# Performance work log

Hardware: AMD Instinct MI355X
Metric: run time of the kernel (lower is better)

The kernel has to match this reference:

```python
import jax, jax.numpy as jnp
import numpy as np

N, NU, R, NX, NY = 16384, 2, 256, 8, 2


def setup_inputs() -> dict:
    key = jax.random.key(0)
    ks = jax.random.split(key, 10)
    A = jax.random.normal(ks[0], (NX, NX), dtype=jnp.float32)
    # scale A to be stable (spectral radius < 1) so the 16k-step recurrence is well-behaved
    rho = jnp.max(jnp.abs(jnp.linalg.eigvals(A.astype(jnp.float32)))).real
    A = (A * (0.95 / rho)).astype(jnp.float32)
    return {
        "u": jax.random.normal(ks[1], (N, NU, R), dtype=jnp.float32),
        "x0": jax.random.normal(ks[2], (NX, R), dtype=jnp.float32),
        "A": A,
        "B_u": jax.random.normal(ks[3], (NX, NU), dtype=jnp.float32),
        "C_y": jax.random.normal(ks[4], (NY, NX), dtype=jnp.float32),
        "D_yu": jax.random.normal(ks[5], (NY, NU), dtype=jnp.float32),
        "u_mean": jax.random.normal(ks[6], (NU,), dtype=jnp.float32),
        "u_std": jax.random.uniform(ks[7], (NU,), dtype=jnp.float32, minval=0.5, maxval=1.5),
        "y_mean": jax.random.normal(ks[8], (NY,), dtype=jnp.float32),
        "y_std": jax.random.uniform(ks[9], (NY,), dtype=jnp.float32, minval=0.5, maxval=1.5),
    }


def reference(u, x0, A, B_u, C_y, D_yu, u_mean, u_std, y_mean, y_std):
    # normalize input as in _simulate_core
    un = (u - u_mean.reshape(1, -1, 1)) / u_std.reshape(1, -1, 1)  # (N, nu, R)

    def step(x, uk):
        # x: (nx, R), uk: (nu, R)
        y = C_y @ x + D_yu @ uk      # (ny, R)
        x_next = A @ x + B_u @ uk    # (nx, R)
        return x_next, (y, x)

    _, (Y, X) = jax.lax.scan(step, x0, un)  # Y: (N, ny, R), X: (N, nx, R)

    # denormalize output
    y = Y * y_std.reshape(1, -1, 1) + y_mean.reshape(1, -1, 1)
    return y, X
```

## Files before the change

kernel.cpp:

```cpp
#include <hip/hip_runtime.h>


#define NSTEPS 16384
#define NUI 2
#define RB 256
#define NXS 8
#define NYO 2
#define L1 64
#define NC1 (NSTEPS / L1)
#define NC2 (NC1 / 2)

__global__ void pow_k(const float* __restrict__ A,
                      float* __restrict__ A64, float* __restrict__ A128) {
    __shared__ float M[64];
    const int t = threadIdx.x;
    const int i = t >> 3, j = t & 7;
    M[t] = A[t];
    __syncthreads();
    for (int it = 0; it < 6; ++it) {
        float acc = 0.f;
        #pragma unroll
        for (int k = 0; k < 8; ++k) acc += M[i * 8 + k] * M[k * 8 + j];
        __syncthreads();
        M[t] = acc;
        __syncthreads();
    }
    A64[t] = M[t];
    float acc = 0.f;
    #pragma unroll
    for (int k = 0; k < 8; ++k) acc += M[i * 8 + k] * M[k * 8 + j];
    A128[t] = acc;
}

__global__ __launch_bounds__(RB) void phase1_k(
    const float* __restrict__ u, const float* __restrict__ A,
    const float* __restrict__ Bu, const float* __restrict__ um,
    const float* __restrict__ us, float* __restrict__ d64) {
    const int c = blockIdx.x;
    const int r = threadIdx.x;
    float a[NXS][NXS];
    #pragma unroll
    for (int i = 0; i < NXS; ++i)
        #pragma unroll
        for (int j = 0; j < NXS; ++j) a[i][j] = A[i * NXS + j];
    float b0[NXS], b1[NXS];
    #pragma unroll
    for (int i = 0; i < NXS; ++i) { b0[i] = Bu[i * NUI]; b1[i] = Bu[i * NUI + 1]; }
    const float um0 = um[0], um1 = um[1];
    const float is0 = 1.0f / us[0], is1 = 1.0f / us[1];
    float t[NXS];
    #pragma unroll
    for (int i = 0; i < NXS; ++i) t[i] = 0.f;
    const float* up = u + (size_t)c * L1 * NUI * RB + r;
    #pragma unroll 4
    for (int j = 0; j < L1; ++j) {
        const float u0 = (up[0]  - um0) * is0;
        const float u1 = (up[RB] - um1) * is1;
        up += NUI * RB;
        float nt[NXS];
        #pragma unroll
        for (int i = 0; i < NXS; ++i) {
            float acc = fmaf(b0[i], u0, b1[i] * u1);
            #pragma unroll
            for (int k = 0; k < NXS; ++k) acc = fmaf(a[i][k], t[k], acc);
            nt[i] = acc;
        }
        #pragma unroll
        for (int i = 0; i < NXS; ++i) t[i] = nt[i];
    }
    float* dp = d64 + (size_t)c * NXS * RB + r;
    #pragma unroll
    for (int i = 0; i < NXS; ++i) dp[i * RB] = t[i];
}

__global__ __launch_bounds__(RB) void combine_k(
    const float* __restrict__ d64, const float* __restrict__ A64,
    float* __restrict__ d128) {
    const int m = blockIdx.x;
    const int r = threadIdx.x;
    float m64[NXS][NXS];
    #pragma unroll
    for (int i = 0; i < NXS; ++i)
        #pragma unroll
        for (int j = 0; j < NXS; ++j) m64[i][j] = A64[i * NXS + j];
    const float* p0 = d64 + (size_t)(2 * m) * NXS * RB + r;
    const float* p1 = p0 + (size_t)NXS * RB;
    float x[NXS], y[NXS];
    #pragma unroll
    for (int i = 0; i < NXS; ++i) { x[i] = p0[i * RB]; y[i] = p1[i * RB]; }
    float* o = d128 + (size_t)m * NXS * RB + r;
    #pragma unroll
    for (int i = 0; i < NXS; ++i) {
        float acc = y[i];
        #pragma unroll
        for (int k = 0; k < NXS; ++k) acc = fmaf(m64[i][k], x[k], acc);
        o[i * RB] = acc;
    }
}

__global__ __launch_bounds__(RB) void phase2_k(
    const float* __restrict__ x0, const float* __restrict__ A128,
    const float* __restrict__ d128, float* __restrict__ s128) {
    const int r = threadIdx.x;
    float m[NXS][NXS];
    #pragma unroll
    for (int i = 0; i < NXS; ++i)
        #pragma unroll
        for (int j = 0; j < NXS; ++j) m[i][j] = A128[i * NXS + j];
    float s[NXS];
    #pragma unroll
    for (int i = 0; i < NXS; ++i) s[i] = x0[i * RB + r];
    float dA[NXS], dB[NXS];
    #pragma unroll
    for (int i = 0; i < NXS; ++i) dA[i] = d128[i * RB + r];
    #pragma unroll
    for (int i = 0; i < NXS; ++i) dB[i] = d128[(size_t)NXS * RB + i * RB + r];
    for (int c = 0; c < NC2; ++c) {
        float* sp = s128 + (size_t)c * NXS * RB + r;
        #pragma unroll
        for (int i = 0; i < NXS; ++i) sp[i * RB] = s[i];
        float dc[NXS];
        #pragma unroll
        for (int i = 0; i < NXS; ++i) dc[i] = dA[i];
        #pragma unroll
        for (int i = 0; i < NXS; ++i) dA[i] = dB[i];
        if (c + 2 < NC2) {
            const float* dp = d128 + (size_t)(c + 2) * NXS * RB + r;
            #pragma unroll
            for (int i = 0; i < NXS; ++i) dB[i] = dp[i * RB];
        }
        float ns[NXS];
        #pragma unroll
        for (int i = 0; i < NXS; ++i) {
            float acc = dc[i];
            #pragma unroll
            for (int k = 0; k < NXS; ++k) acc = fmaf(m[i][k], s[k], acc);
            ns[i] = acc;
        }
        #pragma unroll
        for (int i = 0; i < NXS; ++i) s[i] = ns[i];
    }
}

__global__ __launch_bounds__(RB) void phase3_k(
    const float* __restrict__ u, const float* __restrict__ s128,
    const float* __restrict__ d64, const float* __restrict__ A64,
    const float* __restrict__ A, const float* __restrict__ Bu,
    const float* __restrict__ Cy, const float* __restrict__ Dyu,
    const float* __restrict__ um, const float* __restrict__ us,
    const float* __restrict__ ym, const float* __restrict__ ys,
    float* __restrict__ Y, float* __restrict__ X) {
    const int c = blockIdx.x;
    const int r = threadIdx.x;
    const int m = c >> 1;
    float a[NXS][NXS];
    #pragma unroll
    for (int i = 0; i < NXS; ++i)
        #pragma unroll
        for (int j = 0; j < NXS; ++j) a[i][j] = A[i * NXS + j];
    float b0[NXS], b1[NXS], c0[NXS], c1[NXS];
    #pragma unroll
    for (int i = 0; i < NXS; ++i) { b0[i] = Bu[i * NUI]; b1[i] = Bu[i * NUI + 1]; }
    #pragma unroll
    for (int k = 0; k < NXS; ++k) { c0[k] = Cy[k]; c1[k] = Cy[NXS + k]; }
    const float d00 = Dyu[0], d01 = Dyu[1], d10 = Dyu[2], d11 = Dyu[3];
    const float um0 = um[0], um1 = um[1];
    const float is0 = 1.0f / us[0], is1 = 1.0f / us[1];
    const float ym0 = ym[0], ym1 = ym[1], ys0 = ys[0], ys1 = ys[1];

    const float* sp = s128 + (size_t)m * NXS * RB + r;
    float sv[NXS];
    #pragma unroll
    for (int i = 0; i < NXS; ++i) sv[i] = sp[i * RB];
    float t[NXS];
    if (c & 1) {
        float m64[NXS][NXS];
        #pragma unroll
        for (int i = 0; i < NXS; ++i)
            #pragma unroll
            for (int j = 0; j < NXS; ++j) m64[i][j] = A64[i * NXS + j];
        const float* dp = d64 + (size_t)(c - 1) * NXS * RB + r;
        #pragma unroll
        for (int i = 0; i < NXS; ++i) {
            float acc = dp[i * RB];
            #pragma unroll
            for (int k = 0; k < NXS; ++k) acc = fmaf(m64[i][k], sv[k], acc);
            t[i] = acc;
        }
    } else {
        #pragma unroll
        for (int i = 0; i < NXS; ++i) t[i] = sv[i];
    }

    const float* up = u + (size_t)c * L1 * NUI * RB + r;
    float* Xp = X + (size_t)c * L1 * NXS * RB + r;
    float* Yp = Y + (size_t)c * L1 * NYO * RB + r;
    #pragma unroll 4
    for (int j = 0; j < L1; ++j) {
        const float u0 = (up[0]  - um0) * is0;
        const float u1 = (up[RB] - um1) * is1;
        up += NUI * RB;
        #pragma unroll
        for (int i = 0; i < NXS; ++i) Xp[i * RB] = t[i];
        Xp += NXS * RB;
        float y0 = fmaf(d00, u0, d01 * u1);
        float y1 = fmaf(d10, u0, d11 * u1);
        #pragma unroll
        for (int k = 0; k < NXS; ++k) {
            y0 = fmaf(c0[k], t[k], y0);
            y1 = fmaf(c1[k], t[k], y1);
        }
        Yp[0]  = fmaf(y0, ys0, ym0);
        Yp[RB] = fmaf(y1, ys1, ym1);
        Yp += NYO * RB;
        float nt[NXS];
        #pragma unroll
        for (int i = 0; i < NXS; ++i) {
            float acc = fmaf(b0[i], u0, b1[i] * u1);
            #pragma unroll
            for (int k = 0; k < NXS; ++k) acc = fmaf(a[i][k], t[k], acc);
            nt[i] = acc;
        }
        #pragma unroll
        for (int i = 0; i < NXS; ++i) t[i] = nt[i];
    }
}

extern "C" void kernel_launch(void* const* d_in, const int* in_sizes, int n_in,
                              void* d_out, int out_size, void* d_ws, size_t ws_size,
                              hipStream_t stream) {
    const float* u   = (const float*)d_in[0];
    const float* x0  = (const float*)d_in[1];
    const float* A   = (const float*)d_in[2];
    const float* Bu  = (const float*)d_in[3];
    const float* Cy  = (const float*)d_in[4];
    const float* Dyu = (const float*)d_in[5];
    const float* um  = (const float*)d_in[6];
    const float* us  = (const float*)d_in[7];
    const float* ym  = (const float*)d_in[8];
    const float* ys  = (const float*)d_in[9];

    float* Y = (float*)d_out;
    float* X = Y + (size_t)NSTEPS * NYO * RB;

    float* ws   = (float*)d_ws;
    float* A64  = ws;
    float* A128 = ws + 64;
    float* d64  = ws + 128;
    float* d128 = d64 + (size_t)NC1 * NXS * RB;
    float* s128 = d128 + (size_t)NC2 * NXS * RB;

    pow_k<<<1, 64, 0, stream>>>(A, A64, A128);
    phase1_k<<<NC1, RB, 0, stream>>>(u, A, Bu, um, us, d64);
    combine_k<<<NC2, RB, 0, stream>>>(d64, A64, d128);
    phase2_k<<<1, RB, 0, stream>>>(x0, A128, d128, s128);
    phase3_k<<<NC1, RB, 0, stream>>>(u, s128, d64, A64, A, Bu, Cy, Dyu,
                                     um, us, ym, ys, Y, X);
}
```

Measured before the change: 269.9 us.

## Shorten scan chunks to 32 steps with 4-way combine and wider serial phase

```diff
diff --git a/kernel.cpp b/kernel.cpp
--- a/kernel.cpp
+++ b/kernel.cpp
@@ -6,18 +6,19 @@
 #define RB 256
 #define NXS 8
 #define NYO 2
-#define L1 64
-#define NC1 (NSTEPS / L1)
-#define NC2 (NC1 / 2)
-
-__global__ void pow_k(const float* __restrict__ A,
-                      float* __restrict__ A64, float* __restrict__ A128) {
-    __shared__ float M[64];
+#define LF 32
+#define NC1 (NSTEPS / LF)
+#define NC2 (NC1 / 4)
+
+__global__ void pow_k(const float* __restrict__ A, float* __restrict__ A32,
+                      float* __restrict__ A64, float* __restrict__ A96,
+                      float* __restrict__ A128) {
+    __shared__ float M[64], T32[64];
     const int t = threadIdx.x;
     const int i = t >> 3, j = t & 7;
     M[t] = A[t];
     __syncthreads();
-    for (int it = 0; it < 6; ++it) {
+    for (int it = 0; it < 5; ++it) {
         float acc = 0.f;
         #pragma unroll
         for (int k = 0; k < 8; ++k) acc += M[i * 8 + k] * M[k * 8 + j];
@@ -25,17 +26,31 @@
         M[t] = acc;
         __syncthreads();
     }
+    T32[t] = M[t];
+    A32[t] = M[t];
+    {
+        float acc = 0.f;
+        #pragma unroll
+        for (int k = 0; k < 8; ++k) acc += M[i * 8 + k] * M[k * 8 + j];
+        __syncthreads();
+        M[t] = acc;
+        __syncthreads();
+    }
     A64[t] = M[t];
-    float acc = 0.f;
-    #pragma unroll
-    for (int k = 0; k < 8; ++k) acc += M[i * 8 + k] * M[k * 8 + j];
-    A128[t] = acc;
+    float a96 = 0.f, a128 = 0.f;
+    #pragma unroll
+    for (int k = 0; k < 8; ++k) {
+        a96  += M[i * 8 + k] * T32[k * 8 + j];
+        a128 += M[i * 8 + k] * M[k * 8 + j];
+    }
+    A96[t] = a96;
+    A128[t] = a128;
 }
 
 __global__ __launch_bounds__(RB) void phase1_k(
     const float* __restrict__ u, const float* __restrict__ A,
     const float* __restrict__ Bu, const float* __restrict__ um,
-    const float* __restrict__ us, float* __restrict__ d64) {
+    const float* __restrict__ us, float* __restrict__ d32) {
     const int c = blockIdx.x;
     const int r = threadIdx.x;
     float a[NXS][NXS];
@@ -51,9 +66,9 @@
     float t[NXS];
     #pragma unroll
     for (int i = 0; i < NXS; ++i) t[i] = 0.f;
-    const float* up = u + (size_t)c * L1 * NUI * RB + r;
+    const float* up = u + (size_t)c * LF * NUI * RB + r;
     #pragma unroll 4
-    for (int j = 0; j < L1; ++j) {
+    for (int j = 0; j < LF; ++j) {
         const float u0 = (up[0]  - um0) * is0;
         const float u1 = (up[RB] - um1) * is1;
         up += NUI * RB;
@@ -68,40 +83,53 @@
         #pragma unroll
         for (int i = 0; i < NXS; ++i) t[i] = nt[i];
     }
-    float* dp = d64 + (size_t)c * NXS * RB + r;
+    float* dp = d32 + (size_t)c * NXS * RB + r;
     #pragma unroll
     for (int i = 0; i < NXS; ++i) dp[i * RB] = t[i];
 }
 
-__global__ __launch_bounds__(RB) void combine_k(
-    const float* __restrict__ d64, const float* __restrict__ A64,
+__global__ __launch_bounds__(RB) void combine4_k(
+    const float* __restrict__ d32, const float* __restrict__ A32,
+    const float* __restrict__ A64, const float* __restrict__ A96,
     float* __restrict__ d128) {
     const int m = blockIdx.x;
     const int r = threadIdx.x;
-    float m64[NXS][NXS];
-    #pragma unroll
-    for (int i = 0; i < NXS; ++i)
-        #pragma unroll
-        for (int j = 0; j < NXS; ++j) m64[i][j] = A64[i * NXS + j];
-    const float* p0 = d64 + (size_t)(2 * m) * NXS * RB + r;
-    const float* p1 = p0 + (size_t)NXS * RB;
-    float x[NXS], y[NXS];
-    #pragma unroll
-    for (int i = 0; i < NXS; ++i) { x[i] = p0[i * RB]; y[i] = p1[i * RB]; }
+    float m32[NXS][NXS], m64[NXS][NXS], m96[NXS][NXS];
+    #pragma unroll
+    for (int i = 0; i < NXS; ++i)
+        #pragma unroll
+        for (int j = 0; j < NXS; ++j) {
+            m32[i][j] = A32[i * NXS + j];
+            m64[i][j] = A64[i * NXS + j];
+            m96[i][j] = A96[i * NXS + j];
+        }
+    const float* p = d32 + (size_t)(4 * m) * NXS * RB + r;
+    float x0[NXS], x1[NXS], x2[NXS], x3[NXS];
+    #pragma unroll
+    for (int i = 0; i < NXS; ++i) {
+        x0[i] = p[i * RB];
+        x1[i] = p[(size_t)NXS * RB + i * RB];
+        x2[i] = p[(size_t)2 * NXS * RB + i * RB];
+        x3[i] = p[(size_t)3 * NXS * RB + i * RB];
+    }
     float* o = d128 + (size_t)m * NXS * RB + r;
     #pragma unroll
     for (int i = 0; i < NXS; ++i) {
-        float acc = y[i];
-        #pragma unroll
-        for (int k = 0; k < NXS; ++k) acc = fmaf(m64[i][k], x[k], acc);
+        float acc = x3[i];
+        #pragma unroll
+        for (int k = 0; k < NXS; ++k) {
+            acc = fmaf(m96[i][k], x0[k], acc);
+            acc = fmaf(m64[i][k], x1[k], acc);
+            acc = fmaf(m32[i][k], x2[k], acc);
+        }
         o[i * RB] = acc;
     }
 }
 
-__global__ __launch_bounds__(RB) void phase2_k(
+__global__ __launch_bounds__(64) void phase2_k(
     const float* __restrict__ x0, const float* __restrict__ A128,
     const float* __restrict__ d128, float* __restrict__ s128) {
-    const int r = threadIdx.x;
+    const int r = blockIdx.x * 64 + threadIdx.x;
     float m[NXS][NXS];
     #pragma unroll
     for (int i = 0; i < NXS; ++i)
@@ -110,41 +138,42 @@
     float s[NXS];
     #pragma unroll
     for (int i = 0; i < NXS; ++i) s[i] = x0[i * RB + r];
-    float dA[NXS], dB[NXS];
-    #pragma unroll
-    for (int i = 0; i < NXS; ++i) dA[i] = d128[i * RB + r];
-    #pragma unroll
-    for (int i = 0; i < NXS; ++i) dB[i] = d128[(size_t)NXS * RB + i * RB + r];
-    for (int c = 0; c < NC2; ++c) {
-        float* sp = s128 + (size_t)c * NXS * RB + r;
-        #pragma unroll
-        for (int i = 0; i < NXS; ++i) sp[i * RB] = s[i];
-        float dc[NXS];
-        #pragma unroll
-        for (int i = 0; i < NXS; ++i) dc[i] = dA[i];
-        #pragma unroll
-        for (int i = 0; i < NXS; ++i) dA[i] = dB[i];
-        if (c + 2 < NC2) {
-            const float* dp = d128 + (size_t)(c + 2) * NXS * RB + r;
-            #pragma unroll
-            for (int i = 0; i < NXS; ++i) dB[i] = dp[i * RB];
-        }
-        float ns[NXS];
-        #pragma unroll
-        for (int i = 0; i < NXS; ++i) {
-            float acc = dc[i];
-            #pragma unroll
-            for (int k = 0; k < NXS; ++k) acc = fmaf(m[i][k], s[k], acc);
-            ns[i] = acc;
-        }
-        #pragma unroll
-        for (int i = 0; i < NXS; ++i) s[i] = ns[i];
+    float P[8][NXS];
+    #pragma unroll
+    for (int sl = 0; sl < 8; ++sl) {
+        const float* dp = d128 + (size_t)sl * NXS * RB + r;
+        #pragma unroll
+        for (int i = 0; i < NXS; ++i) P[sl][i] = dp[i * RB];
+    }
+    for (int c = 0; c < NC2; c += 8) {
+        #pragma unroll
+        for (int sl = 0; sl < 8; ++sl) {
+            const int cc = c + sl;
+            float* sp = s128 + (size_t)cc * NXS * RB + r;
+            #pragma unroll
+            for (int i = 0; i < NXS; ++i) sp[i * RB] = s[i];
+            float ns[NXS];
+            #pragma unroll
+            for (int i = 0; i < NXS; ++i) {
+                float acc = P[sl][i];
+                #pragma unroll
+                for (int k = 0; k < NXS; ++k) acc = fmaf(m[i][k], s[k], acc);
+                ns[i] = acc;
+            }
+            if (cc + 8 < NC2) {
+                const float* dp = d128 + (size_t)(cc + 8) * NXS * RB + r;
+                #pragma unroll
+                for (int i = 0; i < NXS; ++i) P[sl][i] = dp[i * RB];
+            }
+            #pragma unroll
+            for (int i = 0; i < NXS; ++i) s[i] = ns[i];
+        }
     }
 }
 
 __global__ __launch_bounds__(RB) void phase3_k(
     const float* __restrict__ u, const float* __restrict__ s128,
-    const float* __restrict__ d64, const float* __restrict__ A64,
+    const float* __restrict__ d32, const float* __restrict__ A32,
     const float* __restrict__ A, const float* __restrict__ Bu,
     const float* __restrict__ Cy, const float* __restrict__ Dyu,
     const float* __restrict__ um, const float* __restrict__ us,
@@ -152,7 +181,8 @@
     float* __restrict__ Y, float* __restrict__ X) {
     const int c = blockIdx.x;
     const int r = threadIdx.x;
-    const int m = c >> 1;
+    const int m = c >> 2;
+    const int p = c & 3;
     float a[NXS][NXS];
     #pragma unroll
     for (int i = 0; i < NXS; ++i)
@@ -168,40 +198,44 @@
     const float is0 = 1.0f / us[0], is1 = 1.0f / us[1];
     const float ym0 = ym[0], ym1 = ym[1], ys0 = ys[0], ys1 = ys[1];
 
-    const float* sp = s128 + (size_t)m * NXS * RB + r;
-    float sv[NXS];
-    #pragma unroll
-    for (int i = 0; i < NXS; ++i) sv[i] = sp[i * RB];
     float t[NXS];
-    if (c & 1) {
-        float m64[NXS][NXS];
+    {
+        const float* sp = s128 + (size_t)m * NXS * RB + r;
+        #pragma unroll
+        for (int i = 0; i < NXS; ++i) t[i] = sp[i * RB];
+    }
+    if (p) {
+        float a32[NXS][NXS];
         #pragma unroll
         for (int i = 0; i < NXS; ++i)
             #pragma unroll
-            for (int j = 0; j < NXS; ++j) m64[i][j] = A64[i * NXS + j];
-        const float* dp = d64 + (size_t)(c - 1) * NXS * RB + r;
-        #pragma unroll
-        for (int i = 0; i < NXS; ++i) {
-            float acc = dp[i * RB];
-            #pragma unroll
-            for (int k = 0; k < NXS; ++k) acc = fmaf(m64[i][k], sv[k], acc);
-            t[i] = acc;
-        }
-    } else {
-        #pragma unroll
-        for (int i = 0; i < NXS; ++i) t[i] = sv[i];
-    }
-
-    const float* up = u + (size_t)c * L1 * NUI * RB + r;
-    float* Xp = X + (size_t)c * L1 * NXS * RB + r;
-    float* Yp = Y + (size_t)c * L1 * NYO * RB + r;
+            for (int j = 0; j < NXS; ++j) a32[i][j] = A32[i * NXS + j];
+        for (int q = 0; q < p; ++q) {
+            const float* dp = d32 + (size_t)(4 * m + q) * NXS * RB + r;
+            float nt[NXS];
+            #pragma unroll
+            for (int i = 0; i < NXS; ++i) {
+                float acc = dp[i * RB];
+                #pragma unroll
+                for (int k = 0; k < NXS; ++k) acc = fmaf(a32[i][k], t[k], acc);
+                nt[i] = acc;
+            }
+            #pragma unroll
+            for (int i = 0; i < NXS; ++i) t[i] = nt[i];
+        }
+    }
+
+    const float* up = u + (size_t)c * LF * NUI * RB + r;
+    float* Xp = X + (size_t)c * LF * NXS * RB + r;
+    float* Yp = Y + (size_t)c * LF * NYO * RB + r;
     #pragma unroll 4
-    for (int j = 0; j < L1; ++j) {
+    for (int j = 0; j < LF; ++j) {
         const float u0 = (up[0]  - um0) * is0;
         const float u1 = (up[RB] - um1) * is1;
         up += NUI * RB;
         #pragma unroll
-        for (int i = 0; i < NXS; ++i) Xp[i * RB] = t[i];
+        for (int i = 0; i < NXS; ++i)
+            __builtin_nontemporal_store(t[i], Xp + i * RB);
         Xp += NXS * RB;
         float y0 = fmaf(d00, u0, d01 * u1);
         float y1 = fmaf(d10, u0, d11 * u1);
@@ -210,8 +244,8 @@
             y0 = fmaf(c0[k], t[k], y0);
             y1 = fmaf(c1[k], t[k], y1);
         }
-        Yp[0]  = fmaf(y0, ys0, ym0);
-        Yp[RB] = fmaf(y1, ys1, ym1);
+        __builtin_nontemporal_store(fmaf(y0, ys0, ym0), Yp);
+        __builtin_nontemporal_store(fmaf(y1, ys1, ym1), Yp + RB);
         Yp += NYO * RB;
         float nt[NXS];
         #pragma unroll
@@ -244,16 +278,18 @@
     float* X = Y + (size_t)NSTEPS * NYO * RB;
 
     float* ws   = (float*)d_ws;
-    float* A64  = ws;
-    float* A128 = ws + 64;
-    float* d64  = ws + 128;
-    float* d128 = d64 + (size_t)NC1 * NXS * RB;
+    float* A32  = ws;
+    float* A64  = ws + 64;
+    float* A96  = ws + 128;
+    float* A128 = ws + 192;
+    float* d32  = ws + 256;
+    float* d128 = d32 + (size_t)NC1 * NXS * RB;
     float* s128 = d128 + (size_t)NC2 * NXS * RB;
 
-    pow_k<<<1, 64, 0, stream>>>(A, A64, A128);
-    phase1_k<<<NC1, RB, 0, stream>>>(u, A, Bu, um, us, d64);
-    combine_k<<<NC2, RB, 0, stream>>>(d64, A64, d128);
-    phase2_k<<<1, RB, 0, stream>>>(x0, A128, d128, s128);
-    phase3_k<<<NC1, RB, 0, stream>>>(u, s128, d64, A64, A, Bu, Cy, Dyu,
+    pow_k<<<1, 64, 0, stream>>>(A, A32, A64, A96, A128);
+    phase1_k<<<NC1, RB, 0, stream>>>(u, A, Bu, um, us, d32);
+    combine4_k<<<NC2, RB, 0, stream>>>(d32, A32, A64, A96, d128);
+    phase2_k<<<4, 64, 0, stream>>>(x0, A128, d128, s128);
+    phase3_k<<<NC1, RB, 0, stream>>>(u, s128, d32, A32, A, Bu, Cy, Dyu,
                                      um, us, ym, ys, Y, X);
 }
```

After: 255.5 us. -5.4%, faster.
